# Performance work log

Measured on AMD Instinct MI355X. Metric: run time of the kernel, lower is better.

## Reference

```python
import jax, jax.numpy as jnp
import numpy as np

ALPHA = 10.0 / 100.0  # dt/tau
RNN_STD = 0.1
NOISE_SCALE = float(np.sqrt(2.0 * (1.0 / ALPHA) * RNN_STD ** 2))


def setup_inputs() -> dict:
    key = jax.random.key(0)
    k0, k1, k2, k3, k4, k5 = jax.random.split(key, 6)
    T, B, I, H, R = 512, 128, 64, 512, 8
    inp = jax.random.normal(k0, (T, B, I), dtype=jnp.float32)
    # input2h Linear params
    W_in = jax.random.normal(k1, (H, I), dtype=jnp.float32) * (1.0 / np.sqrt(I))
    b_in = jax.random.normal(k2, (H,), dtype=jnp.float32) * 0.01
    # kaiming_normal_ fan_in, relu: std = sqrt(2/fan_in); fan_in = dim 1
    U = jax.random.normal(k3, (H, R), dtype=jnp.float32) * np.sqrt(2.0 / R)
    V = jax.random.normal(k4, (R, H), dtype=jnp.float32) * np.sqrt(2.0 / H)
    # pre-scaled recurrent noise, one draw per time step (matches torch loop)
    noise = NOISE_SCALE * jax.random.normal(k5, (T, B, H), dtype=jnp.float32)
    return {"input": inp, "W_in": W_in, "b_in": b_in, "U": U, "V": V, "noise": noise}


def reference(input, W_in, b_in, U, V, noise):
    # Precompute input projection for all steps: (T,B,H)
    x_proj = jnp.einsum('tbi,hi->tbh', input, W_in) + b_in

    def step(h, xs):
        xp, nz = xs
        h = h + nz                       # hidden += noise (pre-scaled)
        rec = (h @ V.T) @ U.T            # low-rank recurrent term: (U @ (V @ h.T)).T
        h_new = jax.nn.relu(xp + rec)
        h = h * (1.0 - ALPHA) + h_new * ALPHA
        return h, h

    B = input.shape[1]
    H = U.shape[0]
    h0 = jnp.zeros((B, H), dtype=input.dtype)
    hN, out = jax.lax.scan(step, h0, (x_proj, noise))
    return out, hN
```

## Files before the change

kernel.cpp:

```cpp
#include <hip/hip_runtime.h>

namespace {

constexpr int T = 512, B = 128, I = 64, H = 512, R = 8;
constexpr int CH = 16;
constexpr int NCH = T / CH;
constexpr float ALPHA = 0.1f;

typedef _Float16 f16x8 __attribute__((ext_vector_type(8)));
typedef float f32x4 __attribute__((ext_vector_type(4)));

#define DPPF(x, ctrl) \
  __int_as_float(__builtin_amdgcn_update_dpp(0, __float_as_int(x), (ctrl), 0xF, 0xF, true))


__global__ __launch_bounds__(512, 1)
void ctrnn(const float* __restrict__ input, const float* __restrict__ W_in,
           const float* __restrict__ b_in, const float* __restrict__ U,
           const float* __restrict__ V, const float* __restrict__ noise,
           float* __restrict__ out) {
  const int b    = blockIdx.x;
  const int tid  = threadIdx.x;
  const int h    = tid;
  const int lane = tid & 63;
  const int wv   = tid >> 6;
  const int l7   = lane & 7;

  __shared__ float lds[CH * H + 2 * 64 + 512];
  float* xp   = lds;
  float* pbuf = lds + CH * H;
  float* dump = pbuf + 128;

  int m = ((lane & 1) << 2) | (lane & 2);
  if (lane & 4) m ^= 7;

  float vperm[8], uperm[8];
  {
    const int sig[8] = {0, 1, 2, 3, 7, 6, 5, 4};
#pragma unroll
    for (int j = 0; j < 8; ++j) vperm[j] = V[(j ^ m) * H + h];
#pragma unroll
    for (int j = 0; j < 8; ++j) uperm[j] = U[h * R + (l7 ^ sig[j])];
  }

  const int colh = 64 * wv + (lane & 15);
  const int krow = (lane >> 4) * 8;
  const int trow = lane & 15;
  f16x8 bfr[4][2];
  float biasf[4];
#pragma unroll
  for (int nt = 0; nt < 4; ++nt) {
    const int hh = colh + 16 * nt;
    biasf[nt] = b_in[hh];
#pragma unroll
    for (int kt = 0; kt < 2; ++kt)
#pragma unroll
      for (int j = 0; j < 8; ++j)
        bfr[nt][kt][j] = (_Float16)W_in[hh * I + kt * 32 + krow + j];
  }

  float hstate = 0.f;
  const int strideTB = B * H;
  const float* noise_b = noise + b * H + h;
  float* out_b = out + b * H + h;

  float ncur[CH], nnxt[CH];
#pragma unroll
  for (int s = 0; s < CH; ++s) ncur[s] = noise_b[s * strideTB];

  float av[2][8];
#pragma unroll
  for (int kt = 0; kt < 2; ++kt) {
    const float* src = input + (trow * B + b) * I + kt * 32 + krow;
    const float4 lo = *(const float4*)src;
    const float4 hi = *(const float4*)(src + 4);
    av[kt][0] = lo.x; av[kt][1] = lo.y; av[kt][2] = lo.z; av[kt][3] = lo.w;
    av[kt][4] = hi.x; av[kt][5] = hi.y; av[kt][6] = hi.z; av[kt][7] = hi.w;
  }

  auto step = [&](int t, int sloc, float nz) {
    const float xpv = xp[sloc * H + h];
    hstate += nz;
    float p0 = vperm[0] * hstate, p1 = vperm[1] * hstate,
          p2 = vperm[2] * hstate, p3 = vperm[3] * hstate,
          p4 = vperm[4] * hstate, p5 = vperm[5] * hstate,
          p6 = vperm[6] * hstate, p7 = vperm[7] * hstate;
    p0 += DPPF(p4, 0xB1); p1 += DPPF(p5, 0xB1);
    p2 += DPPF(p6, 0xB1); p3 += DPPF(p7, 0xB1);
    p0 += DPPF(p2, 0x4E); p1 += DPPF(p3, 0x4E);
    p0 += DPPF(p1, 0x141);
    float sg = p0;
    sg += DPPF(sg, 0x128);
    sg += __shfl_xor(sg, 16, 64);
    sg += __shfl_xor(sg, 32, 64);
    float* wp = (lane < 8) ? (pbuf + (t & 1) * 64 + wv * 8 + m) : (dump + tid);
    *wp = sg;
    __syncthreads();
    float u = pbuf[(t & 1) * 64 + lane];
    u += DPPF(u, 0x128);
    u += __shfl_xor(u, 16, 64);
    u += __shfl_xor(u, 32, 64);
    const float g0 = u;
    const float g1 = DPPF(g0, 0xB1);
    const float g2 = DPPF(g0, 0x4E);
    const float g3 = DPPF(g1, 0x4E);
    const float g4 = DPPF(g0, 0x141);
    const float g5 = DPPF(g1, 0x141);
    const float g6 = DPPF(g2, 0x141);
    const float g7 = DPPF(g3, 0x141);
    float ra = uperm[0] * g0;
    float rb = uperm[4] * g4;
    ra = fmaf(uperm[1], g1, ra);
    rb = fmaf(uperm[5], g5, rb);
    ra = fmaf(uperm[2], g2, ra);
    rb = fmaf(uperm[6], g6, rb);
    ra = fmaf(uperm[3], g3, ra);
    rb = fmaf(uperm[7], g7, rb);
    const float rec = ra + rb;
    float hn = xpv + rec;
    hn = hn > 0.f ? hn : 0.f;
    hstate = fmaf(hstate, 1.f - ALPHA, hn * ALPHA);
    out_b[t * strideTB] = hstate;
  };

  for (int c = 0; c < NCH; ++c) {
    if (c + 1 < NCH) {
      const float* nb = noise_b + (c + 1) * CH * strideTB;
#pragma unroll
      for (int s = 0; s < CH; ++s) nnxt[s] = nb[s * strideTB];
    }
    f16x8 af[2];
#pragma unroll
    for (int kt = 0; kt < 2; ++kt)
#pragma unroll
      for (int j = 0; j < 8; ++j) af[kt][j] = (_Float16)av[kt][j];
#pragma unroll
    for (int nt = 0; nt < 4; ++nt) {
      f32x4 acc = {0.f, 0.f, 0.f, 0.f};
      acc = __builtin_amdgcn_mfma_f32_16x16x32_f16(af[0], bfr[nt][0], acc, 0, 0, 0);
      acc = __builtin_amdgcn_mfma_f32_16x16x32_f16(af[1], bfr[nt][1], acc, 0, 0, 0);
      const int hh = colh + 16 * nt;
      const int t4 = (lane >> 4) * 4;
#pragma unroll
      for (int q = 0; q < 4; ++q) xp[(t4 + q) * H + hh] = acc[q] + biasf[nt];
    }
    if (c + 1 < NCH) {
#pragma unroll
      for (int kt = 0; kt < 2; ++kt) {
        const float* src = input + (((c + 1) * CH + trow) * B + b) * I + kt * 32 + krow;
        const float4 lo = *(const float4*)src;
        const float4 hi = *(const float4*)(src + 4);
        av[kt][0] = lo.x; av[kt][1] = lo.y; av[kt][2] = lo.z; av[kt][3] = lo.w;
        av[kt][4] = hi.x; av[kt][5] = hi.y; av[kt][6] = hi.z; av[kt][7] = hi.w;
      }
    }
    __syncthreads();
    const int tb = c * CH;
#pragma unroll
    for (int s = 0; s < CH; ++s) step(tb + s, s, ncur[s]);
    if (c + 1 < NCH) {
#pragma unroll
      for (int s = 0; s < CH; ++s) ncur[s] = nnxt[s];
    }
  }

  out[T * B * H + b * H + h] = hstate;
}

}

extern "C" void kernel_launch(void* const* d_in, const int* in_sizes, int n_in,
                              void* d_out, int out_size, void* d_ws, size_t ws_size,
                              hipStream_t stream) {
  const float* input = (const float*)d_in[0];
  const float* W_in  = (const float*)d_in[1];
  const float* b_in  = (const float*)d_in[2];
  const float* U     = (const float*)d_in[3];
  const float* V     = (const float*)d_in[4];
  const float* noise = (const float*)d_in[5];
  float* out = (float*)d_out;
  ctrnn<<<dim3(B), dim3(512), 0, stream>>>(input, W_in, b_in, U, V, noise, out);
}
```

Measured before the change: 411.4 us.

## Collapse each batch row onto a single wavefront to remove per-step block barriers

Result: slower. 449.9 us (+9.3%).

```diff
diff --git a/kernel.cpp b/kernel.cpp
--- a/kernel.cpp
+++ b/kernel.cpp
@@ -13,61 +13,58 @@
 #define DPPF(x, ctrl) \
   __int_as_float(__builtin_amdgcn_update_dpp(0, __float_as_int(x), (ctrl), 0xF, 0xF, true))
 
-
-__global__ __launch_bounds__(512, 1)
+__global__ __launch_bounds__(64, 1)
 void ctrnn(const float* __restrict__ input, const float* __restrict__ W_in,
            const float* __restrict__ b_in, const float* __restrict__ U,
            const float* __restrict__ V, const float* __restrict__ noise,
            float* __restrict__ out) {
-  const int b    = blockIdx.x;
-  const int tid  = threadIdx.x;
-  const int h    = tid;
-  const int lane = tid & 63;
-  const int wv   = tid >> 6;
-  const int l7   = lane & 7;
+  const int b = blockIdx.x;
+  const int L = threadIdx.x;
 
-  __shared__ float lds[CH * H + 2 * 64 + 512];
-  float* xp   = lds;
-  float* pbuf = lds + CH * H;
-  float* dump = pbuf + 128;
+  __shared__ __align__(16) _Float16 Wl[H * I];
+  __shared__ __align__(16) float xp[CH * H];
 
-  int m = ((lane & 1) << 2) | (lane & 2);
-  if (lane & 4) m ^= 7;
-
-  float vperm[8], uperm[8];
-  {
-    const int sig[8] = {0, 1, 2, 3, 7, 6, 5, 4};
-#pragma unroll
-    for (int j = 0; j < 8; ++j) vperm[j] = V[(j ^ m) * H + h];
-#pragma unroll
-    for (int j = 0; j < 8; ++j) uperm[j] = U[h * R + (l7 ^ sig[j])];
+  for (int rr = 0; rr < 64; ++rr) {
+    const int bid = rr * 64 + L;
+    const int h = bid >> 3, ib = (bid & 7) * 8;
+    const float* src = W_in + h * I + ib;
+    const float4 lo = *(const float4*)src;
+    const float4 hi = *(const float4*)(src + 4);
+    f16x8 v;
+    v[0] = (_Float16)lo.x; v[1] = (_Float16)lo.y; v[2] = (_Float16)lo.z; v[3] = (_Float16)lo.w;
+    v[4] = (_Float16)hi.x; v[5] = (_Float16)hi.y; v[6] = (_Float16)hi.z; v[7] = (_Float16)hi.w;
+    *(f16x8*)&Wl[h * I + (ib ^ ((h & 7) << 3))] = v;
   }
 
-  const int colh = 64 * wv + (lane & 15);
-  const int krow = (lane >> 4) * 8;
-  const int trow = lane & 15;
-  f16x8 bfr[4][2];
-  float biasf[4];
+  int m = ((L & 1) << 2) | (L & 2);
+  if (L & 4) m ^= 7;
+
+  const int ss[8] = {0, 4, 2, 6, 1, 5, 3, 7};
+  float Vr[8][8], Up[8][8], bia[8], hs[8];
 #pragma unroll
-  for (int nt = 0; nt < 4; ++nt) {
-    const int hh = colh + 16 * nt;
-    biasf[nt] = b_in[hh];
+  for (int j = 0; j < 8; ++j)
 #pragma unroll
-    for (int kt = 0; kt < 2; ++kt)
+    for (int k = 0; k < 8; ++k) Vr[j][k] = V[(j ^ m) * H + 8 * L + k];
 #pragma unroll
-      for (int j = 0; j < 8; ++j)
-        bfr[nt][kt][j] = (_Float16)W_in[hh * I + kt * 32 + krow + j];
+  for (int k = 0; k < 8; ++k) {
+    bia[k] = b_in[8 * L + k];
+    hs[k] = 0.f;
+#pragma unroll
+    for (int j = 0; j < 8; ++j) Up[k][j] = U[(8 * L + k) * R + (m ^ ss[j])];
   }
 
-  float hstate = 0.f;
-  const int strideTB = B * H;
-  const float* noise_b = noise + b * H + h;
-  float* out_b = out + b * H + h;
+  const int BH = B * H;
+  const float* nz_b = noise + b * H + 8 * L;
+  float* out_b = out + b * H + 8 * L;
 
-  float ncur[CH], nnxt[CH];
+  float4 nb0[4], nb1[4];
 #pragma unroll
-  for (int s = 0; s < CH; ++s) ncur[s] = noise_b[s * strideTB];
+  for (int s = 0; s < 4; ++s) {
+    nb0[s] = *(const float4*)(nz_b + s * BH);
+    nb1[s] = *(const float4*)(nz_b + s * BH + 4);
+  }
 
+  const int trow = L & 15, krow = (L >> 4) * 8;
   float av[2][8];
 #pragma unroll
   for (int kt = 0; kt < 2; ++kt) {
@@ -78,71 +75,21 @@
     av[kt][4] = hi.x; av[kt][5] = hi.y; av[kt][6] = hi.z; av[kt][7] = hi.w;
   }
 
-  auto step = [&](int t, int sloc, float nz) {
-    const float xpv = xp[sloc * H + h];
-    hstate += nz;
-    float p0 = vperm[0] * hstate, p1 = vperm[1] * hstate,
-          p2 = vperm[2] * hstate, p3 = vperm[3] * hstate,
-          p4 = vperm[4] * hstate, p5 = vperm[5] * hstate,
-          p6 = vperm[6] * hstate, p7 = vperm[7] * hstate;
-    p0 += DPPF(p4, 0xB1); p1 += DPPF(p5, 0xB1);
-    p2 += DPPF(p6, 0xB1); p3 += DPPF(p7, 0xB1);
-    p0 += DPPF(p2, 0x4E); p1 += DPPF(p3, 0x4E);
-    p0 += DPPF(p1, 0x141);
-    float sg = p0;
-    sg += DPPF(sg, 0x128);
-    sg += __shfl_xor(sg, 16, 64);
-    sg += __shfl_xor(sg, 32, 64);
-    float* wp = (lane < 8) ? (pbuf + (t & 1) * 64 + wv * 8 + m) : (dump + tid);
-    *wp = sg;
-    __syncthreads();
-    float u = pbuf[(t & 1) * 64 + lane];
-    u += DPPF(u, 0x128);
-    u += __shfl_xor(u, 16, 64);
-    u += __shfl_xor(u, 32, 64);
-    const float g0 = u;
-    const float g1 = DPPF(g0, 0xB1);
-    const float g2 = DPPF(g0, 0x4E);
-    const float g3 = DPPF(g1, 0x4E);
-    const float g4 = DPPF(g0, 0x141);
-    const float g5 = DPPF(g1, 0x141);
-    const float g6 = DPPF(g2, 0x141);
-    const float g7 = DPPF(g3, 0x141);
-    float ra = uperm[0] * g0;
-    float rb = uperm[4] * g4;
-    ra = fmaf(uperm[1], g1, ra);
-    rb = fmaf(uperm[5], g5, rb);
-    ra = fmaf(uperm[2], g2, ra);
-    rb = fmaf(uperm[6], g6, rb);
-    ra = fmaf(uperm[3], g3, ra);
-    rb = fmaf(uperm[7], g7, rb);
-    const float rec = ra + rb;
-    float hn = xpv + rec;
-    hn = hn > 0.f ? hn : 0.f;
-    hstate = fmaf(hstate, 1.f - ALPHA, hn * ALPHA);
-    out_b[t * strideTB] = hstate;
-  };
-
   for (int c = 0; c < NCH; ++c) {
-    if (c + 1 < NCH) {
-      const float* nb = noise_b + (c + 1) * CH * strideTB;
+    f16x8 af0, af1;
 #pragma unroll
-      for (int s = 0; s < CH; ++s) nnxt[s] = nb[s * strideTB];
-    }
-    f16x8 af[2];
+    for (int j = 0; j < 8; ++j) { af0[j] = (_Float16)av[0][j]; af1[j] = (_Float16)av[1][j]; }
 #pragma unroll
-    for (int kt = 0; kt < 2; ++kt)
+    for (int nt = 0; nt < 32; ++nt) {
+      const int h0 = nt * 16 + trow;
+      const int sw = (h0 & 7) << 3;
+      const f16x8 b0 = *(const f16x8*)&Wl[h0 * I + (krow ^ sw)];
+      const f16x8 b1 = *(const f16x8*)&Wl[h0 * I + ((32 + krow) ^ sw)];
+      f32x4 acc = {0.f, 0.f, 0.f, 0.f};
+      acc = __builtin_amdgcn_mfma_f32_16x16x32_f16(af0, b0, acc, 0, 0, 0);
+      acc = __builtin_amdgcn_mfma_f32_16x16x32_f16(af1, b1, acc, 0, 0, 0);
 #pragma unroll
-      for (int j = 0; j < 8; ++j) af[kt][j] = (_Float16)av[kt][j];
-#pragma unroll
-    for (int nt = 0; nt < 4; ++nt) {
-      f32x4 acc = {0.f, 0.f, 0.f, 0.f};
-      acc = __builtin_amdgcn_mfma_f32_16x16x32_f16(af[0], bfr[nt][0], acc, 0, 0, 0);
-      acc = __builtin_amdgcn_mfma_f32_16x16x32_f16(af[1], bfr[nt][1], acc, 0, 0, 0);
-      const int hh = colh + 16 * nt;
-      const int t4 = (lane >> 4) * 4;
-#pragma unroll
-      for (int q = 0; q < 4; ++q) xp[(t4 + q) * H + hh] = acc[q] + biasf[nt];
+      for (int q = 0; q < 4; ++q) xp[((L >> 4) * 4 + q) * H + h0] = acc[q];
     }
     if (c + 1 < NCH) {
 #pragma unroll
@@ -154,17 +101,63 @@
         av[kt][4] = hi.x; av[kt][5] = hi.y; av[kt][6] = hi.z; av[kt][7] = hi.w;
       }
     }
-    __syncthreads();
+
     const int tb = c * CH;
+    for (int s4 = 0; s4 < CH; s4 += 4) {
 #pragma unroll
-    for (int s = 0; s < CH; ++s) step(tb + s, s, ncur[s]);
-    if (c + 1 < NCH) {
+      for (int u = 0; u < 4; ++u) {
+        const int s = s4 + u, t = tb + s;
+        const float4 n0 = nb0[u], n1 = nb1[u];
+        int tp = t + 4; if (tp > T - 1) tp = T - 1;
+        nb0[u] = *(const float4*)(nz_b + tp * BH);
+        nb1[u] = *(const float4*)(nz_b + tp * BH + 4);
+        hs[0] += n0.x; hs[1] += n0.y; hs[2] += n0.z; hs[3] += n0.w;
+        hs[4] += n1.x; hs[5] += n1.y; hs[6] += n1.z; hs[7] += n1.w;
+        float p[8];
 #pragma unroll
-      for (int s = 0; s < CH; ++s) ncur[s] = nnxt[s];
+        for (int j = 0; j < 8; ++j) {
+          p[j] = Vr[j][0] * hs[0];
+#pragma unroll
+          for (int k = 1; k < 8; ++k) p[j] = fmaf(Vr[j][k], hs[k], p[j]);
+        }
+        p[0] += DPPF(p[4], 0xB1); p[1] += DPPF(p[5], 0xB1);
+        p[2] += DPPF(p[6], 0xB1); p[3] += DPPF(p[7], 0xB1);
+        p[0] += DPPF(p[2], 0x4E); p[1] += DPPF(p[3], 0x4E);
+        p[0] += DPPF(p[1], 0x141);
+        float sg = p[0];
+        sg += DPPF(sg, 0x128);
+        sg += __shfl_xor(sg, 16, 64);
+        sg += __shfl_xor(sg, 32, 64);
+        float g[8];
+        g[0] = sg;
+        g[1] = DPPF(g[0], 0xB1); g[2] = DPPF(g[0], 0x4E); g[3] = DPPF(g[1], 0x4E);
+        g[4] = DPPF(g[0], 0x141); g[5] = DPPF(g[1], 0x141);
+        g[6] = DPPF(g[2], 0x141); g[7] = DPPF(g[3], 0x141);
+        const float4 x0 = *(const float4*)&xp[s * H + 8 * L];
+        const float4 x1 = *(const float4*)&xp[s * H + 8 * L + 4];
+        const float xv[8] = {x0.x, x0.y, x0.z, x0.w, x1.x, x1.y, x1.z, x1.w};
+#pragma unroll
+        for (int k = 0; k < 8; ++k) {
+          float rec = Up[k][0] * g[0];
+#pragma unroll
+          for (int j = 1; j < 8; ++j) rec = fmaf(Up[k][j], g[j], rec);
+          float hn = xv[k] + bia[k] + rec;
+          hn = hn > 0.f ? hn : 0.f;
+          hs[k] = fmaf(hs[k], 1.f - ALPHA, hn * ALPHA);
+        }
+        const float4 o0 = {hs[0], hs[1], hs[2], hs[3]};
+        const float4 o1 = {hs[4], hs[5], hs[6], hs[7]};
+        *(float4*)(out_b + t * BH) = o0;
+        *(float4*)(out_b + t * BH + 4) = o1;
+      }
     }
   }
 
-  out[T * B * H + b * H + h] = hstate;
+  float* hN = out + (size_t)T * BH + b * H + 8 * L;
+  const float4 o0 = {hs[0], hs[1], hs[2], hs[3]};
+  const float4 o1 = {hs[4], hs[5], hs[6], hs[7]};
+  *(float4*)(hN) = o0;
+  *(float4*)(hN + 4) = o1;
 }
 
 }
@@ -179,5 +172,5 @@
   const float* V     = (const float*)d_in[4];
   const float* noise = (const float*)d_in[5];
   float* out = (float*)d_out;
-  ctrnn<<<dim3(B), dim3(512), 0, stream>>>(input, W_in, b_in, U, V, noise, out);
+  ctrnn<<<dim3(B), dim3(64), 0, stream>>>(input, W_in, b_in, U, V, noise, out);
 }
```
